# Kernel tuning notes

Hardware: AMD Instinct MI355X
Metric: run time of the kernel (lower is better)

Reference implementation:

```python
import jax, jax.numpy as jnp
import numpy as np

B, T = 64, 2048
QD, KD, VD, AD = 512, 512, 512, 256


def setup_inputs() -> dict:
    key = jax.random.key(0)
    ks = jax.random.split(key, 9)
    s = lambda d: 1.0 / np.sqrt(d)
    return {
        "query": jax.random.normal(ks[0], (B, QD), jnp.float32),
        "key": jax.random.normal(ks[1], (B, T, KD), jnp.float32),
        "value": jax.random.normal(ks[2], (B, T, VD), jnp.float32),
        "Wq": jax.random.uniform(ks[3], (QD, AD), jnp.float32, -s(QD), s(QD)),
        "bq": jax.random.uniform(ks[4], (AD,), jnp.float32, -s(QD), s(QD)),
        "Wk": jax.random.uniform(ks[5], (KD, AD), jnp.float32, -s(KD), s(KD)),
        "bk": jax.random.uniform(ks[6], (AD,), jnp.float32, -s(KD), s(KD)),
        "Wo": jax.random.uniform(ks[7], (AD, 1), jnp.float32, -s(AD), s(AD)),
        "bo": jax.random.uniform(ks[8], (1,), jnp.float32, -s(AD), s(AD)),
    }


def reference(query, key, value, Wq, bq, Wk, bk, Wo, bo):
    # q_proj: [B, 1, AD]; k_proj: [B, T, AD]
    q_proj = (query @ Wq + bq)[:, None, :]
    k_proj = jnp.einsum("btk,ka->bta", key, Wk) + bk
    # score: [B, T, 1]
    score = jnp.tanh(q_proj + k_proj) @ Wo + bo
    attn = jax.nn.softmax(score, axis=1)  # softmax over keys (dim 1)
    # context: [B, VD] = sum_t attn[b,t] * value[b,t,:]
    context = jnp.einsum("bt,btv->bv", attn[..., 0], value)
    return context, attn[..., 0]
```

## Files before the change

kernel.cpp:

```cpp
#include <hip/hip_runtime.h>

#define NB 64
#define NT 2048
#define NQD 512
#define NKD 512
#define NVD 512
#define NAD 256

typedef __attribute__((ext_vector_type(8))) short s16x8;
typedef __attribute__((ext_vector_type(4))) float fx4;
typedef __attribute__((ext_vector_type(4))) unsigned int u32x4;

__device__ __forceinline__ short f2bf(float x) {
  union { float f; unsigned u; } v; v.f = x;
  return (short)((v.u + 0x7fffu + ((v.u >> 16) & 1u)) >> 16);
}

__device__ __forceinline__ unsigned cvt_pk_bf16(float lo, float hi) {
  unsigned r;
  asm("v_cvt_pk_bf16_f32 %0, %1, %2" : "=v"(r) : "v"(lo), "v"(hi));
  return r;
}

__device__ __forceinline__ float fast_tanh(float x) {
  float e = __expf(x + x);
  return 1.0f - 2.0f * __builtin_amdgcn_rcpf(e + 1.0f);
}

__global__ void prep_kernel(const float* __restrict__ query, const float* __restrict__ Wq,
                            const float* __restrict__ bq, const float* __restrict__ bk,
                            const float* __restrict__ Wk,
                            float* __restrict__ qpk, short* __restrict__ Bpk) {
  __shared__ float q[NQD];
  const int tid = threadIdx.x;
  if (blockIdx.x < NB) {
    const int b = blockIdx.x;
    for (int k = tid; k < NQD; k += 256) q[k] = query[b * NQD + k];
    __syncthreads();
    float acc = bq[tid] + bk[tid];
#pragma unroll 8
    for (int k = 0; k < NQD; ++k) acc += q[k] * Wq[k * NAD + tid];
    qpk[b * NAD + tid] = acc;
  } else {
    const int ks = blockIdx.x - NB;
#pragma unroll
    for (int rep = 0; rep < 4; ++rep) {
      const int o = rep * 256 + tid;
      const int wnt = o >> 6;
      const int l = o & 63;
      const int g = l >> 4, h = l & 15;
      const int n = wnt * 16 + h;
      const int k0 = ks * 32 + g * 8;
      s16x8 v;
#pragma unroll
      for (int j = 0; j < 8; ++j) v[j] = f2bf(Wk[(size_t)(k0 + j) * NAD + n]);
      *(s16x8*)(Bpk + (size_t)(ks * 1024 + o) * 8) = v;
    }
  }
}

__global__ void __launch_bounds__(256, 2)
score_kernel(const float* __restrict__ key, const short* __restrict__ Bpk,
             const float* __restrict__ qpk, const float* __restrict__ Wo,
             float* __restrict__ score) {
  __shared__ short As[64 * 512];
  __shared__ float sred[4][64];
  const int tid = threadIdx.x;
  const int w = tid >> 6, l = tid & 63;
  const int g = l >> 4, h = l & 15;
  const int m0 = blockIdx.x * 64;
  const int b = m0 >> 11;

  const short* bbase = Bpk + (size_t)(w * 256 + l) * 8;

  s16x8 bcur[4], bn1[4];
#pragma unroll
  for (int nt = 0; nt < 4; ++nt) bcur[nt] = *(const s16x8*)(bbase + nt * 512);
#pragma unroll
  for (int nt = 0; nt < 4; ++nt) bn1[nt] = *(const s16x8*)(bbase + 8192 + nt * 512);

  {
    const float* tile = key + (size_t)m0 * NKD;
#pragma unroll
    for (int j = 0; j < 16; ++j) {
      const int c = tid + j * 256;
      const float* gp = tile + c * 8;
      fx4 x0 = *(const fx4*)gp;
      fx4 x1 = *(const fx4*)(gp + 4);
      u32x4 pw;
      pw[0] = cvt_pk_bf16(x0[0], x0[1]);
      pw[1] = cvt_pk_bf16(x0[2], x0[3]);
      pw[2] = cvt_pk_bf16(x1[0], x1[1]);
      pw[3] = cvt_pk_bf16(x1[2], x1[3]);
      const int row = c >> 6, col = c & 63;
      *(u32x4*)((char*)As + ((row * 1024 + col * 16) ^ ((row & 7) << 4))) = pw;
    }
  }
  __syncthreads();

  fx4 acc[4][4];
#pragma unroll
  for (int i = 0; i < 4; ++i)
#pragma unroll
    for (int j = 0; j < 4; ++j) acc[i][j] = fx4{0.f, 0.f, 0.f, 0.f};

  int abase[4];
#pragma unroll
  for (int mt = 0; mt < 4; ++mt) abase[mt] = (mt * 16 + h) * 1024 + g * 16;
  const int sw = (h & 7) << 4;

#pragma unroll 2
  for (int ks = 0; ks < 16; ++ks) {
    s16x8 bn2[4];
    if (ks < 14) {
#pragma unroll
      for (int nt = 0; nt < 4; ++nt)
        bn2[nt] = *(const s16x8*)(bbase + (size_t)(ks + 2) * 8192 + nt * 512);
    }
    s16x8 af[4];
#pragma unroll
    for (int mt = 0; mt < 4; ++mt)
      af[mt] = *(const s16x8*)((const char*)As + ((abase[mt] + ks * 64) ^ sw));
#pragma unroll
    for (int mt = 0; mt < 4; ++mt)
#pragma unroll
      for (int nt = 0; nt < 4; ++nt)
        acc[mt][nt] = __builtin_amdgcn_mfma_f32_16x16x32_bf16(af[mt], bcur[nt], acc[mt][nt], 0, 0, 0);
#pragma unroll
    for (int nt = 0; nt < 4; ++nt) bcur[nt] = bn1[nt];
    if (ks < 14) {
#pragma unroll
      for (int nt = 0; nt < 4; ++nt) bn1[nt] = bn2[nt];
    }
  }

  float qv[4], wv[4];
#pragma unroll
  for (int nt = 0; nt < 4; ++nt) {
    const int n = w * 64 + nt * 16 + h;
    qv[nt] = qpk[b * NAD + n];
    wv[nt] = Wo[n];
  }
#pragma unroll
  for (int mt = 0; mt < 4; ++mt) {
#pragma unroll
    for (int rr = 0; rr < 4; ++rr) {
      float s = fast_tanh(acc[mt][0][rr] + qv[0]) * wv[0]
              + fast_tanh(acc[mt][1][rr] + qv[1]) * wv[1]
              + fast_tanh(acc[mt][2][rr] + qv[2]) * wv[2]
              + fast_tanh(acc[mt][3][rr] + qv[3]) * wv[3];
#pragma unroll
      for (int off = 1; off < 16; off <<= 1) s += __shfl_xor(s, off, 64);
      if (h == 0) sred[w][mt * 16 + g * 4 + rr] = s;
    }
  }
  __syncthreads();
  if (tid < 64)
    score[m0 + tid] = sred[0][tid] + sred[1][tid] + sred[2][tid] + sred[3][tid];
}

__global__ void softmax_kernel(const float* __restrict__ score, float* __restrict__ attn) {
  __shared__ float redm[4];
  __shared__ float reds[4];
  const int b = blockIdx.x, tid = threadIdx.x;
  const float* s = score + (size_t)b * NT;
  float v[8];
  float m = -3.0e38f;
#pragma unroll
  for (int j = 0; j < 8; ++j) { v[j] = s[tid + j * 256]; m = fmaxf(m, v[j]); }
#pragma unroll
  for (int off = 1; off < 64; off <<= 1) m = fmaxf(m, __shfl_xor(m, off, 64));
  if ((tid & 63) == 0) redm[tid >> 6] = m;
  __syncthreads();
  m = fmaxf(fmaxf(redm[0], redm[1]), fmaxf(redm[2], redm[3]));
  float sum = 0.f;
#pragma unroll
  for (int j = 0; j < 8; ++j) { v[j] = __expf(v[j] - m); sum += v[j]; }
#pragma unroll
  for (int off = 1; off < 64; off <<= 1) sum += __shfl_xor(sum, off, 64);
  if ((tid & 63) == 0) reds[tid >> 6] = sum;
  __syncthreads();
  sum = reds[0] + reds[1] + reds[2] + reds[3];
  const float inv = 1.0f / sum;
#pragma unroll
  for (int j = 0; j < 8; ++j) attn[(size_t)b * NT + tid + j * 256] = v[j] * inv;
}

__global__ void ctx_partial_kernel(const float* __restrict__ attn, const float* __restrict__ value,
                                   float* __restrict__ partial) {
  __shared__ float a[64];
  __shared__ fx4 red[128];
  const int blk = blockIdx.x;
  const int b = blk >> 5, tc = blk & 31;
  const int tid = threadIdx.x;
  if (tid < 64) a[tid] = attn[(size_t)b * NT + tc * 64 + tid];
  __syncthreads();
  const int half = tid >> 7;
  const int vi = (tid & 127) * 4;
  const float* vp = value + ((size_t)b * NT + tc * 64 + half) * NVD + vi;
  fx4 s = fx4{0.f, 0.f, 0.f, 0.f};
#pragma unroll 8
  for (int t = 0; t < 64; t += 2) {
    fx4 x = *(const fx4*)(vp + (size_t)t * NVD);
    const float wt = a[t + half];
    s += x * wt;
  }
  if (half) red[tid & 127] = s;
  __syncthreads();
  if (!half) {
    s += red[tid];
    *(fx4*)(partial + (size_t)blk * NVD + vi) = s;
  }
}

__global__ void ctx_reduce_kernel(const float* __restrict__ partial, float* __restrict__ ctx) {
  const int i = blockIdx.x * 256 + threadIdx.x;
  const int b = i >> 9, v = i & (NVD - 1);
  float s = 0.f;
#pragma unroll
  for (int tc = 0; tc < 32; ++tc) s += partial[(size_t)(b * 32 + tc) * NVD + v];
  ctx[i] = s;
}

extern "C" void kernel_launch(void* const* d_in, const int* in_sizes, int n_in,
                              void* d_out, int out_size, void* d_ws, size_t ws_size,
                              hipStream_t stream) {
  const float* query = (const float*)d_in[0];
  const float* key   = (const float*)d_in[1];
  const float* value = (const float*)d_in[2];
  const float* Wq    = (const float*)d_in[3];
  const float* bq    = (const float*)d_in[4];
  const float* Wk    = (const float*)d_in[5];
  const float* bk    = (const float*)d_in[6];
  const float* Wo    = (const float*)d_in[7];

  float* out  = (float*)d_out;
  float* ctx  = out;
  float* attn = out + NB * NVD;

  char* ws = (char*)d_ws;
  float* qpk     = (float*)(ws);
  short* Bpk     = (short*)(ws + 64 * 1024);
  float* score   = (float*)(ws + (64 + 256) * 1024);
  float* partial = (float*)(ws + (64 + 256 + 512) * 1024);

  prep_kernel<<<NB + 16, 256, 0, stream>>>(query, Wq, bq, bk, Wk, qpk, Bpk);
  score_kernel<<<(NB * NT) / 64, 256, 0, stream>>>(key, Bpk, qpk, Wo, score);
  softmax_kernel<<<NB, 256, 0, stream>>>(score, attn);
  ctx_partial_kernel<<<NB * 32, 256, 0, stream>>>(attn, value, partial);
  ctx_reduce_kernel<<<(NB * NVD) / 256, 256, 0, stream>>>(partial, ctx);
}
```

Measured before the change: 171.1 us.

## Double-buffer key tiles via direct global-to-LDS loads in score kernel

The score kernel no longer loads its whole 64x512 key tile into registers, converts it to bf16 and writes it to LDS before computing. It now streams 64-column fp32 chunks into a double-buffered LDS ring with global_load_lds, so the load of the next chunk overlaps the MFMA work on the current one. Conversion to bf16 moves to after the LDS read, and the smaller LDS footprint lets launch bounds rise to 3 blocks per CU. In exchange the per-MFMA conversion work grows, each chunk now needs a barrier, and LDS read traffic doubles because the data is stored as fp32.

Result: faster. 156.5 us (-8.5%).

```diff
diff --git a/kernel.cpp b/kernel.cpp
--- a/kernel.cpp
+++ b/kernel.cpp
@@ -25,6 +25,12 @@
 __device__ __forceinline__ float fast_tanh(float x) {
   float e = __expf(x + x);
   return 1.0f - 2.0f * __builtin_amdgcn_rcpf(e + 1.0f);
+}
+
+__device__ __forceinline__ void gload_lds16(const void* g, void* l) {
+  __builtin_amdgcn_global_load_lds(
+      (const __attribute__((address_space(1))) unsigned int*)g,
+      (__attribute__((address_space(3))) unsigned int*)l, 16, 0, 0);
 }
 
 __global__ void prep_kernel(const float* __restrict__ query, const float* __restrict__ Wq,
@@ -59,11 +65,11 @@
   }
 }
 
-__global__ void __launch_bounds__(256, 2)
+__global__ void __launch_bounds__(256, 3)
 score_kernel(const float* __restrict__ key, const short* __restrict__ Bpk,
              const float* __restrict__ qpk, const float* __restrict__ Wo,
              float* __restrict__ score) {
-  __shared__ short As[64 * 512];
+  __shared__ float As[2][64 * 64];
   __shared__ float sred[4][64];
   const int tid = threadIdx.x;
   const int w = tid >> 6, l = tid & 63;
@@ -79,59 +85,72 @@
 #pragma unroll
   for (int nt = 0; nt < 4; ++nt) bn1[nt] = *(const s16x8*)(bbase + 8192 + nt * 512);
 
-  {
-    const float* tile = key + (size_t)m0 * NKD;
-#pragma unroll
-    for (int j = 0; j < 16; ++j) {
-      const int c = tid + j * 256;
-      const float* gp = tile + c * 8;
-      fx4 x0 = *(const fx4*)gp;
-      fx4 x1 = *(const fx4*)(gp + 4);
-      u32x4 pw;
-      pw[0] = cvt_pk_bf16(x0[0], x0[1]);
-      pw[1] = cvt_pk_bf16(x0[2], x0[3]);
-      pw[2] = cvt_pk_bf16(x1[0], x1[1]);
-      pw[3] = cvt_pk_bf16(x1[2], x1[3]);
-      const int row = c >> 6, col = c & 63;
-      *(u32x4*)((char*)As + ((row * 1024 + col * 16) ^ ((row & 7) << 4))) = pw;
+  const float* srcp[4];
+  int ldsoff[4];
+#pragma unroll
+  for (int i = 0; i < 4; ++i) {
+    const int p = w * 256 + i * 64 + l;
+    const int row = p >> 4, c = p & 15;
+    srcp[i] = key + (size_t)(m0 + row) * NKD + ((c ^ (row & 15)) << 2);
+    ldsoff[i] = w * 4096 + i * 1024;
+  }
+
+  auto stage = [&](int bb, int ck) {
+#pragma unroll
+    for (int i = 0; i < 4; ++i)
+      gload_lds16(srcp[i] + ck * 64, (char*)&As[bb][0] + ldsoff[i]);
+  };
+
+  stage(0, 0);
+  __syncthreads();
+
+  fx4 acc[4][4];
+#pragma unroll
+  for (int i = 0; i < 4; ++i)
+#pragma unroll
+    for (int j = 0; j < 4; ++j) acc[i][j] = fx4{0.f, 0.f, 0.f, 0.f};
+
+  int buf = 0;
+  for (int ck = 0; ck < 8; ++ck) {
+    if (ck < 7) stage(buf ^ 1, ck + 1);
+#pragma unroll
+    for (int kl = 0; kl < 2; ++kl) {
+      const int ks = ck * 2 + kl;
+      s16x8 bn2[4];
+      if (ks < 14) {
+#pragma unroll
+        for (int nt = 0; nt < 4; ++nt)
+          bn2[nt] = *(const s16x8*)(bbase + (size_t)(ks + 2) * 8192 + nt * 512);
+      }
+      s16x8 af[4];
+#pragma unroll
+      for (int mt = 0; mt < 4; ++mt) {
+        const int R = mt * 16 + h;
+        const int c0 = kl * 8 + g * 2;
+        const char* base = (const char*)&As[buf][0] + R * 256;
+        fx4 lo = *(const fx4*)(base + (((c0    ) ^ h) << 4));
+        fx4 hi = *(const fx4*)(base + (((c0 + 1) ^ h) << 4));
+        u32x4 uu;
+        uu[0] = cvt_pk_bf16(lo[0], lo[1]);
+        uu[1] = cvt_pk_bf16(lo[2], lo[3]);
+        uu[2] = cvt_pk_bf16(hi[0], hi[1]);
+        uu[3] = cvt_pk_bf16(hi[2], hi[3]);
+        af[mt] = *(s16x8*)&uu;
+      }
+#pragma unroll
+      for (int mt = 0; mt < 4; ++mt)
+#pragma unroll
+        for (int nt = 0; nt < 4; ++nt)
+          acc[mt][nt] = __builtin_amdgcn_mfma_f32_16x16x32_bf16(af[mt], bcur[nt], acc[mt][nt], 0, 0, 0);
+#pragma unroll
+      for (int nt = 0; nt < 4; ++nt) bcur[nt] = bn1[nt];
+      if (ks < 14) {
+#pragma unroll
+        for (int nt = 0; nt < 4; ++nt) bn1[nt] = bn2[nt];
+      }
     }
-  }
-  __syncthreads();
-
-  fx4 acc[4][4];
-#pragma unroll
-  for (int i = 0; i < 4; ++i)
-#pragma unroll
-    for (int j = 0; j < 4; ++j) acc[i][j] = fx4{0.f, 0.f, 0.f, 0.f};
-
-  int abase[4];
-#pragma unroll
-  for (int mt = 0; mt < 4; ++mt) abase[mt] = (mt * 16 + h) * 1024 + g * 16;
-  const int sw = (h & 7) << 4;
-
-#pragma unroll 2
-  for (int ks = 0; ks < 16; ++ks) {
-    s16x8 bn2[4];
-    if (ks < 14) {
-#pragma unroll
-      for (int nt = 0; nt < 4; ++nt)
-        bn2[nt] = *(const s16x8*)(bbase + (size_t)(ks + 2) * 8192 + nt * 512);
-    }
-    s16x8 af[4];
-#pragma unroll
-    for (int mt = 0; mt < 4; ++mt)
-      af[mt] = *(const s16x8*)((const char*)As + ((abase[mt] + ks * 64) ^ sw));
-#pragma unroll
-    for (int mt = 0; mt < 4; ++mt)
-#pragma unroll
-      for (int nt = 0; nt < 4; ++nt)
-        acc[mt][nt] = __builtin_amdgcn_mfma_f32_16x16x32_bf16(af[mt], bcur[nt], acc[mt][nt], 0, 0, 0);
-#pragma unroll
-    for (int nt = 0; nt < 4; ++nt) bcur[nt] = bn1[nt];
-    if (ks < 14) {
-#pragma unroll
-      for (int nt = 0; nt < 4; ++nt) bn1[nt] = bn2[nt];
-    }
+    __syncthreads();
+    buf ^= 1;
   }
 
   float qv[4], wv[4];
```
